# Kernel tuning notes

Measured on AMD Instinct MI355X. Metric: run time of the kernel, lower is better.

The kernel has to match this reference:

```python
import jax, jax.numpy as jnp
import numpy as np

B, T, H = 4096, 256, 64  # batch, seq_len, hidden_size


def _lstm_layer(x, W_ih, W_hh, b_ih, b_hh):
    """One LSTM layer, batch_first. x: [B,T,D]; W_ih: [4H,D]; W_hh: [4H,H].
    PyTorch gate order: i, f, g, o."""
    Bb = x.shape[0]
    Hh = W_hh.shape[1]
    # Precompute input contribution for all timesteps: [B,T,4H]
    gx = jnp.einsum('btd,gd->btg', x, W_ih) + b_ih + b_hh

    def step(carry, g_t):
        h, c = carry
        g = g_t + h @ W_hh.T  # [B,4H]
        i, f, gg, o = jnp.split(g, 4, axis=-1)
        i = jax.nn.sigmoid(i)
        f = jax.nn.sigmoid(f)
        gg = jnp.tanh(gg)
        o = jax.nn.sigmoid(o)
        c = f * c + i * gg
        h = o * jnp.tanh(c)
        return (h, c), h

    h0 = jnp.zeros((Bb, Hh), x.dtype)
    c0 = jnp.zeros((Bb, Hh), x.dtype)
    _, hs = jax.lax.scan(step, (h0, c0), jnp.swapaxes(gx, 0, 1))  # hs: [T,B,H]
    return jnp.swapaxes(hs, 0, 1)  # [B,T,H]


def setup_inputs() -> dict:
    key = jax.random.key(0)
    ks = jax.random.split(key, 11)
    s = 1.0 / np.sqrt(H)  # keep recurrent dynamics well-scaled
    return {
        'recipe': jax.random.normal(ks[0], (B, T, 1), jnp.float32),
        'W_ih0': jax.random.normal(ks[1], (4 * H, 1), jnp.float32) * s,
        'W_hh0': jax.random.normal(ks[2], (4 * H, H), jnp.float32) * s,
        'b_ih0': jax.random.normal(ks[3], (4 * H,), jnp.float32) * s,
        'b_hh0': jax.random.normal(ks[4], (4 * H,), jnp.float32) * s,
        'W_ih1': jax.random.normal(ks[5], (4 * H, H), jnp.float32) * s,
        'W_hh1': jax.random.normal(ks[6], (4 * H, H), jnp.float32) * s,
        'b_ih1': jax.random.normal(ks[7], (4 * H,), jnp.float32) * s,
        'b_hh1': jax.random.normal(ks[8], (4 * H,), jnp.float32) * s,
        'W_lin': jax.random.normal(ks[9], (H, H), jnp.float32) * s,
        'b_lin': jax.random.normal(ks[10], (H,), jnp.float32) * s,
    }


def reference(recipe, W_ih0, W_hh0, b_ih0, b_hh0, W_ih1, W_hh1, b_ih1, b_hh1, W_lin, b_lin):
    h1 = _lstm_layer(recipe, W_ih0, W_hh0, b_ih0, b_hh0)  # [B,T,H]
    h2 = _lstm_layer(h1, W_ih1, W_hh1, b_ih1, b_hh1)      # [B,T,H]
    return h2[:, -1, :] @ W_lin.T + b_lin                   # [B,H]
```

## Files before the change

### kernel.cpp

```cpp
#include <hip/hip_runtime.h>

typedef _Float16 v8h __attribute__((ext_vector_type(8)));
typedef float    v4f __attribute__((ext_vector_type(4)));

#define MFMA16(A,B,C) __builtin_amdgcn_mfma_f32_16x16x32_f16((A),(B),(C),0,0,0)

#define RPB 16
#define TT  256
#define HH  64
#define KST 136
#define SG  256.0f
#define TG  512.0f
#define IOFF 4096.5f
#define TSC2 -2.88539008f

__global__ __launch_bounds__(512, 2)
void lstm2_kernel(const float* __restrict__ x,
                  const float* __restrict__ Wih0,
                  const float* __restrict__ Whh0,
                  const float* __restrict__ bih0,
                  const float* __restrict__ bhh0,
                  const float* __restrict__ Wih1,
                  const float* __restrict__ Whh1,
                  const float* __restrict__ bih1,
                  const float* __restrict__ bhh1,
                  const float* __restrict__ Wlin,
                  const float* __restrict__ blin,
                  float* __restrict__ out)
{
    __shared__ float xl[TT][RPB];
    __shared__ __align__(16) _Float16 hs[2][RPB][KST];
    __shared__ float hbF[RPB][HH];
    __shared__ float lutS[8192];
    __shared__ float lutT[8192];

    const int tid  = threadIdx.x;
    const int w    = tid >> 6;
    const int l15  = tid & 15;
    const int q    = (tid & 63) >> 4;
    const int row0 = (int)blockIdx.x * RPB;
    const int jj   = (w & 3) * 16 + l15;
    const bool isA = (w < 4);
    const int  mr  = q * 4;

    for (int idx = tid; idx < RPB * TT; idx += 512) {
        int m = idx & 15, t = idx >> 4;
        xl[t][m] = x[(row0 + m) * TT + t];
    }
    for (int idx = tid; idx < 2 * RPB * KST; idx += 512)
        ((_Float16*)hs)[idx] = (_Float16)0.f;
    for (int i = tid; i < 8192; i += 512) {
        float e = __expf(-(i - 4096) * (1.0f / 256.0f));
        lutS[i] = 1.0f / (1.0f + e);
        lutT[i] = 2.0f / (1.0f + e) - 1.0f;
    }

    auto lutSv = [&](float F) -> float {
        F = __builtin_amdgcn_fmed3f(F, 0.0f, 8191.0f);
        return lutS[(int)F];
    };
    auto lutTv = [&](float F) -> float {
        F = __builtin_amdgcn_fmed3f(F, 0.0f, 8191.0f);
        return lutT[(int)F];
    };
    auto tanhf_fast = [&](float c) -> float {
        return fmaf(2.f, __builtin_amdgcn_rcpf(1.f + __builtin_exp2f(c * TSC2)), -1.f);
    };

    float wi0s[4], b0s[4];
    v8h   wh0[4][2];
    v4f   b1v[4];
    v8h   wi1[4][2], wh1[4][2];
    if (isA) {
        #pragma unroll
        for (int tau = 0; tau < 4; tau++) {
            float sc = (tau == 2) ? TG : SG;
            int n = tau * 64 + jj;
            wi0s[tau] = Wih0[n] * sc;
            b0s[tau]  = (bih0[n] + bhh0[n]) * sc + IOFF;
            #pragma unroll
            for (int kk = 0; kk < 2; kk++) {
                int k0 = kk * 32 + q * 8;
                v8h a;
                #pragma unroll
                for (int j = 0; j < 8; j++)
                    a[j] = (_Float16)(Whh0[n * HH + k0 + j] * sc);
                wh0[tau][kk] = a;
            }
        }
    } else {
        #pragma unroll
        for (int tau = 0; tau < 4; tau++) {
            float sc = (tau == 2) ? TG : SG;
            int n = tau * 64 + jj;
            float b1 = (bih1[n] + bhh1[n]) * sc + IOFF;
            b1v[tau] = (v4f){b1, b1, b1, b1};
            #pragma unroll
            for (int kk = 0; kk < 2; kk++) {
                int k0 = kk * 32 + q * 8;
                v8h b, c;
                #pragma unroll
                for (int j = 0; j < 8; j++) {
                    b[j] = (_Float16)(Wih1[n * HH + k0 + j] * sc);
                    c[j] = (_Float16)(Whh1[n * HH + k0 + j] * sc);
                }
                wi1[tau][kk] = b; wh1[tau][kk] = c;
            }
        }
    }

    float cs[4] = {0.f, 0.f, 0.f, 0.f};
    __syncthreads();

    if (isA) {
        #pragma unroll
        for (int r = 0; r < 4; r++) {
            int m = mr + r;
            float xv = xl[0][m];
            float iv = lutSv(fmaf(xv, wi0s[0], b0s[0]));
            float gv = lutTv(fmaf(xv, wi0s[2], b0s[2]));
            float ov = lutSv(fmaf(xv, wi0s[3], b0s[3]));
            cs[r] = iv * gv;
            hs[0][m][jj] = (_Float16)(ov * tanhf_fast(cs[r]));
        }
    }
    __syncthreads();

    auto step = [&](int k, int p, int pw, bool last) {
        float sv[4][4];
        if (isA) {
            v8h a0 = *(const v8h*)&hs[p][l15][q * 8];
            v8h a1 = *(const v8h*)&hs[p][l15][32 + q * 8];
            int kx = (k < TT) ? k : (TT - 1);
            v4f xv = *(const v4f*)&xl[kx][mr];

            #pragma unroll
            for (int tau = 0; tau < 4; tau++) {
                v4f acc;
                #pragma unroll
                for (int r = 0; r < 4; r++)
                    acc[r] = fmaf(xv[r], wi0s[tau], b0s[tau]);
                __builtin_amdgcn_s_setprio(1);
                acc = MFMA16(a0, wh0[tau][0], acc);
                acc = MFMA16(a1, wh0[tau][1], acc);
                __builtin_amdgcn_s_setprio(0);
                if (tau == 2) {
                    #pragma unroll
                    for (int r = 0; r < 4; r++) sv[tau][r] = lutTv(acc[r]);
                } else {
                    #pragma unroll
                    for (int r = 0; r < 4; r++) sv[tau][r] = lutSv(acc[r]);
                }
            }
            _Float16* wp = &hs[pw][mr][jj];
            #pragma unroll
            for (int r = 0; r < 4; r++) {
                float iv = sv[0][r], fv = sv[1][r];
                float gv = sv[2][r], ov = sv[3][r];
                cs[r] = fmaf(fv, cs[r], iv * gv);
                wp[r * KST] = (_Float16)(ov * tanhf_fast(cs[r]));
            }
        } else {
            v8h a0 = *(const v8h*)&hs[p][l15][q * 8];
            v8h a1 = *(const v8h*)&hs[p][l15][32 + q * 8];
            v8h b0 = *(const v8h*)&hs[p][l15][64 + q * 8];
            v8h b1 = *(const v8h*)&hs[p][l15][96 + q * 8];

            #pragma unroll
            for (int tau = 0; tau < 4; tau++) {
                __builtin_amdgcn_s_setprio(1);
                v4f acc = MFMA16(a0, wi1[tau][0], b1v[tau]);
                acc = MFMA16(a1, wi1[tau][1], acc);
                acc = MFMA16(b0, wh1[tau][0], acc);
                acc = MFMA16(b1, wh1[tau][1], acc);
                __builtin_amdgcn_s_setprio(0);
                if (tau == 2) {
                    #pragma unroll
                    for (int r = 0; r < 4; r++) sv[tau][r] = lutTv(acc[r]);
                } else {
                    #pragma unroll
                    for (int r = 0; r < 4; r++) sv[tau][r] = lutSv(acc[r]);
                }
            }
            _Float16* wp = &hs[pw][mr][64 + jj];
            #pragma unroll
            for (int r = 0; r < 4; r++) {
                float iv = sv[0][r], fv = sv[1][r];
                float gv = sv[2][r], ov = sv[3][r];
                cs[r] = fmaf(fv, cs[r], iv * gv);
                float hv = ov * tanhf_fast(cs[r]);
                wp[r * KST] = (_Float16)hv;
                if (last) hbF[mr + r][jj] = hv;
            }
        }
        __syncthreads();
    };

    for (int k = 1; k <= TT; k += 2) {
        step(k,     0, 1, false);
        step(k + 1, 1, 0, (k + 1) == TT);
    }

    int m  = tid >> 5;
    int n0 = (tid & 31) * 2;
    float a0o = blin[n0], a1o = blin[n0 + 1];
    #pragma unroll 8
    for (int j = 0; j < HH; j++) {
        float h = hbF[m][j];
        a0o = fmaf(h, Wlin[(n0 + 0) * HH + j], a0o);
        a1o = fmaf(h, Wlin[(n0 + 1) * HH + j], a1o);
    }
    out[(row0 + m) * HH + n0]     = a0o;
    out[(row0 + m) * HH + n0 + 1] = a1o;
}

extern "C" void kernel_launch(void* const* d_in, const int* in_sizes, int n_in,
                              void* d_out, int out_size, void* d_ws, size_t ws_size,
                              hipStream_t stream) {
    const float* x    = (const float*)d_in[0];
    const float* Wih0 = (const float*)d_in[1];
    const float* Whh0 = (const float*)d_in[2];
    const float* bih0 = (const float*)d_in[3];
    const float* bhh0 = (const float*)d_in[4];
    const float* Wih1 = (const float*)d_in[5];
    const float* Whh1 = (const float*)d_in[6];
    const float* bih1 = (const float*)d_in[7];
    const float* bhh1 = (const float*)d_in[8];
    const float* Wlin = (const float*)d_in[9];
    const float* blin = (const float*)d_in[10];
    lstm2_kernel<<<256, 512, 0, stream>>>(x, Wih0, Whh0, bih0, bhh0,
                                          Wih1, Whh1, bih1, bhh1,
                                          Wlin, blin, (float*)d_out);
}
```

Before: 270.6 us.

## Halve rows per block to launch twice as many blocks across CUs

Each block now handles 8 batch rows instead of 16, and the grid is doubled to 512 blocks. The MFMA 16-row tiles are filled by duplicating 8 rows (l7 indexing), and each lane post-processes only 2 of the 4 accumulator rows. This trades wasted MFMA work and duplicate LUT setup per block for more parallelism across the 256 CUs, which shortens the serial recurrence per CU. The final linear layer is remapped to one output per thread.

After: 384.8 us. +42.2%, slower.

```diff
diff --git a/kernel.cpp b/kernel.cpp
--- a/kernel.cpp
+++ b/kernel.cpp
@@ -5,7 +5,7 @@
 
 #define MFMA16(A,B,C) __builtin_amdgcn_mfma_f32_16x16x32_f16((A),(B),(C),0,0,0)
 
-#define RPB 16
+#define RPB 8
 #define TT  256
 #define HH  64
 #define KST 136
@@ -28,7 +28,7 @@
                   const float* __restrict__ blin,
                   float* __restrict__ out)
 {
-    __shared__ float xl[TT][RPB];
+    __shared__ __align__(16) float xl[TT][RPB];
     __shared__ __align__(16) _Float16 hs[2][RPB][KST];
     __shared__ float hbF[RPB][HH];
     __shared__ float lutS[8192];
@@ -37,14 +37,17 @@
     const int tid  = threadIdx.x;
     const int w    = tid >> 6;
     const int l15  = tid & 15;
+    const int l7   = tid & 7;
     const int q    = (tid & 63) >> 4;
     const int row0 = (int)blockIdx.x * RPB;
     const int jj   = (w & 3) * 16 + l15;
     const bool isA = (w < 4);
-    const int  mr  = q * 4;
+    const int  ro  = (q >> 1) * 2;
+    const int  mr  = (q & 1) * 4 + ro;
+    const int  xrb = (q & 1) * 4;
 
     for (int idx = tid; idx < RPB * TT; idx += 512) {
-        int m = idx & 15, t = idx >> 4;
+        int m = idx >> 8, t = idx & 255;
         xl[t][m] = x[(row0 + m) * TT + t];
     }
     for (int idx = tid; idx < 2 * RPB * KST; idx += 512)
@@ -109,30 +112,30 @@
         }
     }
 
-    float cs[4] = {0.f, 0.f, 0.f, 0.f};
+    float cs[2] = {0.f, 0.f};
     __syncthreads();
 
     if (isA) {
         #pragma unroll
-        for (int r = 0; r < 4; r++) {
-            int m = mr + r;
+        for (int i = 0; i < 2; i++) {
+            int m = mr + i;
             float xv = xl[0][m];
             float iv = lutSv(fmaf(xv, wi0s[0], b0s[0]));
             float gv = lutTv(fmaf(xv, wi0s[2], b0s[2]));
             float ov = lutSv(fmaf(xv, wi0s[3], b0s[3]));
-            cs[r] = iv * gv;
-            hs[0][m][jj] = (_Float16)(ov * tanhf_fast(cs[r]));
+            cs[i] = iv * gv;
+            hs[0][m][jj] = (_Float16)(ov * tanhf_fast(cs[i]));
         }
     }
     __syncthreads();
 
     auto step = [&](int k, int p, int pw, bool last) {
-        float sv[4][4];
+        float sv[4][2];
         if (isA) {
-            v8h a0 = *(const v8h*)&hs[p][l15][q * 8];
-            v8h a1 = *(const v8h*)&hs[p][l15][32 + q * 8];
+            v8h a0 = *(const v8h*)&hs[p][l7][q * 8];
+            v8h a1 = *(const v8h*)&hs[p][l7][32 + q * 8];
             int kx = (k < TT) ? k : (TT - 1);
-            v4f xv = *(const v4f*)&xl[kx][mr];
+            v4f xv = *(const v4f*)&xl[kx][xrb];
 
             #pragma unroll
             for (int tau = 0; tau < 4; tau++) {
@@ -146,25 +149,25 @@
                 __builtin_amdgcn_s_setprio(0);
                 if (tau == 2) {
                     #pragma unroll
-                    for (int r = 0; r < 4; r++) sv[tau][r] = lutTv(acc[r]);
+                    for (int i = 0; i < 2; i++) sv[tau][i] = lutTv(acc[ro + i]);
                 } else {
                     #pragma unroll
-                    for (int r = 0; r < 4; r++) sv[tau][r] = lutSv(acc[r]);
+                    for (int i = 0; i < 2; i++) sv[tau][i] = lutSv(acc[ro + i]);
                 }
             }
             _Float16* wp = &hs[pw][mr][jj];
             #pragma unroll
-            for (int r = 0; r < 4; r++) {
-                float iv = sv[0][r], fv = sv[1][r];
-                float gv = sv[2][r], ov = sv[3][r];
-                cs[r] = fmaf(fv, cs[r], iv * gv);
-                wp[r * KST] = (_Float16)(ov * tanhf_fast(cs[r]));
+            for (int i = 0; i < 2; i++) {
+                float iv = sv[0][i], fv = sv[1][i];
+                float gv = sv[2][i], ov = sv[3][i];
+                cs[i] = fmaf(fv, cs[i], iv * gv);
+                wp[i * KST] = (_Float16)(ov * tanhf_fast(cs[i]));
             }
         } else {
-            v8h a0 = *(const v8h*)&hs[p][l15][q * 8];
-            v8h a1 = *(const v8h*)&hs[p][l15][32 + q * 8];
-            v8h b0 = *(const v8h*)&hs[p][l15][64 + q * 8];
-            v8h b1 = *(const v8h*)&hs[p][l15][96 + q * 8];
+            v8h a0 = *(const v8h*)&hs[p][l7][q * 8];
+            v8h a1 = *(const v8h*)&hs[p][l7][32 + q * 8];
+            v8h b0 = *(const v8h*)&hs[p][l7][64 + q * 8];
+            v8h b1 = *(const v8h*)&hs[p][l7][96 + q * 8];
 
             #pragma unroll
             for (int tau = 0; tau < 4; tau++) {
@@ -176,21 +179,21 @@
                 __builtin_amdgcn_s_setprio(0);
                 if (tau == 2) {
                     #pragma unroll
-                    for (int r = 0; r < 4; r++) sv[tau][r] = lutTv(acc[r]);
+                    for (int i = 0; i < 2; i++) sv[tau][i] = lutTv(acc[ro + i]);
                 } else {
                     #pragma unroll
-                    for (int r = 0; r < 4; r++) sv[tau][r] = lutSv(acc[r]);
+                    for (int i = 0; i < 2; i++) sv[tau][i] = lutSv(acc[ro + i]);
                 }
             }
             _Float16* wp = &hs[pw][mr][64 + jj];
             #pragma unroll
-            for (int r = 0; r < 4; r++) {
-                float iv = sv[0][r], fv = sv[1][r];
-                float gv = sv[2][r], ov = sv[3][r];
-                cs[r] = fmaf(fv, cs[r], iv * gv);
-                float hv = ov * tanhf_fast(cs[r]);
-                wp[r * KST] = (_Float16)hv;
-                if (last) hbF[mr + r][jj] = hv;
+            for (int i = 0; i < 2; i++) {
+                float iv = sv[0][i], fv = sv[1][i];
+                float gv = sv[2][i], ov = sv[3][i];
+                cs[i] = fmaf(fv, cs[i], iv * gv);
+                float hv = ov * tanhf_fast(cs[i]);
+                wp[i * KST] = (_Float16)hv;
+                if (last) hbF[mr + i][jj] = hv;
             }
         }
         __syncthreads();
@@ -201,17 +204,13 @@
         step(k + 1, 1, 0, (k + 1) == TT);
     }
 
-    int m  = tid >> 5;
-    int n0 = (tid & 31) * 2;
-    float a0o = blin[n0], a1o = blin[n0 + 1];
+    int m = tid >> 6;
+    int n = tid & 63;
+    float ao = blin[n];
     #pragma unroll 8
-    for (int j = 0; j < HH; j++) {
-        float h = hbF[m][j];
-        a0o = fmaf(h, Wlin[(n0 + 0) * HH + j], a0o);
-        a1o = fmaf(h, Wlin[(n0 + 1) * HH + j], a1o);
-    }
-    out[(row0 + m) * HH + n0]     = a0o;
-    out[(row0 + m) * HH + n0 + 1] = a1o;
+    for (int j = 0; j < HH; j++)
+        ao = fmaf(hbF[m][j], Wlin[n * HH + j], ao);
+    out[(row0 + m) * HH + n] = ao;
 }
 
 extern "C" void kernel_launch(void* const* d_in, const int* in_sizes, int n_in,
@@ -228,7 +227,7 @@
     const float* bhh1 = (const float*)d_in[8];
     const float* Wlin = (const float*)d_in[9];
     const float* blin = (const float*)d_in[10];
-    lstm2_kernel<<<256, 512, 0, stream>>>(x, Wih0, Whh0, bih0, bhh0,
+    lstm2_kernel<<<512, 512, 0, stream>>>(x, Wih0, Whh0, bih0, bhh0,
                                           Wih1, Whh1, bih1, bhh1,
                                           Wlin, blin, (float*)d_out);
 }
```
